# Optimization experiments

Measured on AMD Instinct MI355X. Metric: run time of the kernel, lower is better.

## Reference

```python
import jax, jax.numpy as jnp
import numpy as np
import math

B, S, D, H = 8, 1024, 512, 8  # batch, seqlen, d_model, heads
DK = D // H

def setup_inputs() -> dict:
    key = jax.random.key(0)
    ks = jax.random.split(key, 8)
    std = 1.0 / math.sqrt(D)
    return {
        "x": jax.random.normal(ks[0], (B, S, D), jnp.float32),
        "utT_similarities": jax.random.uniform(ks[1], (B, S, S), jnp.float32),
        "Wk": jax.random.normal(ks[2], (D, D), jnp.float32) * std,
        "bk": jnp.zeros((D,), jnp.float32),
        "Wv": jax.random.normal(ks[3], (D, D), jnp.float32) * std,
        "bv": jnp.zeros((D,), jnp.float32),
        "Wo": jax.random.normal(ks[4], (D, D), jnp.float32) * std,
        "bo": jnp.zeros((D,), jnp.float32),
        "gammas": jax.random.normal(ks[5], (H, 1, 1), jnp.float32) * 0.1,
    }

def reference(x, utT_similarities, Wk, bk, Wv, bv, Wo, bo, gammas):
    b, s, d = x.shape
    h = gammas.shape[0]
    dk = d // h
    NEG = -1e32

    def split_heads(t):  # [b,s,d] -> [b,h,s,dk]
        return t.reshape(b, s, h, dk).transpose(0, 2, 1, 3)

    # kq_same=True: q and k share k_linear
    q = split_heads(x @ Wk.T + bk)
    k = q
    v = split_heads(x @ Wv.T + bv)

    scores = jnp.einsum('bhid,bhjd->bhij', q, k) / jnp.sqrt(jnp.float32(dk))
    scores = scores * utT_similarities[:, None, :, :]

    mask = jnp.tril(jnp.ones((s, s), dtype=bool))  # causal, incl diagonal (mask=1)

    # distance-decay block (no_grad in torch -> stop_gradient)
    s_ = jax.nn.softmax(jnp.where(mask, scores, NEG), axis=-1) * mask
    distcum = jnp.cumsum(s_, axis=-1)
    disttotal = jnp.sum(s_, axis=-1, keepdims=True)
    idx = jnp.arange(s)
    position_effect = jnp.abs(idx[None, :] - idx[:, None]).astype(jnp.float32)  # [s,s]
    dist_scores = jnp.sqrt(jnp.clip((disttotal - distcum) * position_effect, 0.0, None))
    dist_scores = jax.lax.stop_gradient(dist_scores)

    gamma = -jax.nn.softplus(gammas)[None]  # [1,h,1,1]
    total_effect = jnp.clip(jnp.exp(dist_scores * gamma), 1e-5, 1e5)

    scores = jax.nn.softmax(jnp.where(mask, scores * total_effect, NEG), axis=-1)
    # zero_pad=False (mask=1 path), dropout is identity in eval
    out = jnp.einsum('bhij,bhjd->bhid', scores, v)
    out = out.transpose(0, 2, 1, 3).reshape(b, s, d)
    return out @ Wo.T + bo
```

## Files before the change

### kernel.cpp

```cpp
#include <hip/hip_runtime.h>
#include <math.h>

#define NB   8
#define SS   1024
#define DD   512
#define HH   8
#define DKK  64
#define NEGF (-3.0e38f)

#define QSTR 88
#define SSTR 257
#define PSTR 280

typedef _Float16 half8 __attribute__((ext_vector_type(8)));
typedef float    f32x4 __attribute__((ext_vector_type(4)));

#define GLDS16(g, l) __builtin_amdgcn_global_load_lds( \
    (const __attribute__((address_space(1))) void*)(g), \
    (__attribute__((address_space(3))) void*)(l), 16, 0, 0)

__global__ __launch_bounds__(256) void cvt_fp16(
    const float* __restrict__ x,  _Float16* __restrict__ xh,
    const float* __restrict__ wk, _Float16* __restrict__ wkh,
    const float* __restrict__ wv, _Float16* __restrict__ wvh,
    const float* __restrict__ wo, _Float16* __restrict__ woh)
{
    const size_t NX = (size_t)NB * SS * DD;
    const size_t NW = (size_t)DD * DD;
    size_t f = ((size_t)blockIdx.x * 256 + threadIdx.x) * 8;
    const float* src; _Float16* dst; size_t off;
    if (f < NX)               { src = x;  dst = xh;  off = f; }
    else if (f < NX + NW)     { src = wk; dst = wkh; off = f - NX; }
    else if (f < NX + 2*NW)   { src = wv; dst = wvh; off = f - NX - 2*NW + NW; }
    else                      { src = wo; dst = woh; off = f - NX - 2*NW; }
    float4 f0 = *(const float4*)&src[off];
    float4 f1 = *(const float4*)&src[off + 4];
    half8 hv = {(_Float16)f0.x,(_Float16)f0.y,(_Float16)f0.z,(_Float16)f0.w,
                (_Float16)f1.x,(_Float16)f1.y,(_Float16)f1.z,(_Float16)f1.w};
    *(half8*)&dst[off] = hv;
}

__global__ __launch_bounds__(256) void gemm_qv(
    const _Float16* __restrict__ xh,
    const _Float16* __restrict__ wkh, const float* __restrict__ bk,
    const _Float16* __restrict__ wvh, const float* __restrict__ bv,
    _Float16* __restrict__ q_ws, _Float16* __restrict__ vt_ws)
{
    __shared__ __align__(16) _Float16 Ah[128 * 32];
    __shared__ __align__(16) _Float16 Bh[128 * 32];

    const int m0  = blockIdx.x * 128;
    const int n0c = blockIdx.y * 128;
    const bool is_v = (n0c >= DD);
    const _Float16* __restrict__ Wp = is_v ? wvh : wkh;
    const float*    __restrict__ bp = is_v ? bv : bk;
    const int n0 = n0c & (DD - 1);

    const int tid  = threadIdx.x;
    const int w    = tid >> 6;
    const int lane = tid & 63;
    const int quad = lane >> 4;
    const int n    = lane & 15;
    const int wm   = w >> 1, wn = w & 1;

    const int ci0 = (w * 2 + 0) * 64 + lane;
    const int ci1 = (w * 2 + 1) * 64 + lane;
    const int r0c = ci0 >> 2, c0c = (ci0 & 3) * 8;
    const int r1c = ci1 >> 2, c1c = (ci1 & 3) * 8;
    _Float16* ldsA0 = &Ah[(w * 2 + 0) * 512];
    _Float16* ldsA1 = &Ah[(w * 2 + 1) * 512];
    _Float16* ldsB0 = &Bh[(w * 2 + 0) * 512];
    _Float16* ldsB1 = &Bh[(w * 2 + 1) * 512];

    f32x4 acc[4][4] = {};

    for (int k0 = 0; k0 < DD; k0 += 32) {
        __syncthreads();
        GLDS16(&xh[(size_t)(m0 + r0c) * DD + k0 + c0c], ldsA0);
        GLDS16(&xh[(size_t)(m0 + r1c) * DD + k0 + c1c], ldsA1);
        GLDS16(&Wp[(size_t)(n0 + r0c) * DD + k0 + c0c], ldsB0);
        GLDS16(&Wp[(size_t)(n0 + r1c) * DD + k0 + c1c], ldsB1);
        __syncthreads();
        half8 af[4], bf[4];
        #pragma unroll
        for (int mi = 0; mi < 4; ++mi)
            af[mi] = *(const half8*)&Ah[(wm*64 + mi*16 + n) * 32 + quad*8];
        #pragma unroll
        for (int ni = 0; ni < 4; ++ni)
            bf[ni] = *(const half8*)&Bh[(wn*64 + ni*16 + n) * 32 + quad*8];
        #pragma unroll
        for (int mi = 0; mi < 4; ++mi)
            #pragma unroll
            for (int ni = 0; ni < 4; ++ni)
                acc[mi][ni] = __builtin_amdgcn_mfma_f32_16x16x32_f16(
                    af[mi], bf[ni], acc[mi][ni], 0, 0, 0);
    }

    #pragma unroll
    for (int mi = 0; mi < 4; ++mi) {
        #pragma unroll
        for (int ni = 0; ni < 4; ++ni) {
            const int col = n0 + wn*64 + ni*16 + n;
            const int h   = col >> 6;
            const int dk  = col & 63;
            const float bias = bp[col];
            const int gbase = m0 + wm*64 + mi*16 + quad*4;
            const int bidx  = gbase >> 10;
            const int sr    = gbase & (SS - 1);
            if (!is_v) {
                #pragma unroll
                for (int reg = 0; reg < 4; ++reg)
                    q_ws[((size_t)(bidx * HH + h) * SS + sr + reg) * DKK + dk] =
                        (_Float16)(acc[mi][ni][reg] + bias);
            } else {
                _Float16 h4[4];
                #pragma unroll
                for (int reg = 0; reg < 4; ++reg)
                    h4[reg] = (_Float16)(acc[mi][ni][reg] + bias);
                *(uint2*)&vt_ws[((size_t)(bidx * HH + h) * DKK + dk) * SS + sr] =
                    *(uint2*)h4;
            }
        }
    }
}

__global__ __launch_bounds__(256) void gemm_out(
    const _Float16* __restrict__ A,
    const _Float16* __restrict__ woh, const float* __restrict__ bo,
    float* __restrict__ out)
{
    __shared__ __align__(16) _Float16 Ah[128 * 32];
    __shared__ __align__(16) _Float16 Bh[128 * 32];

    const int m0 = blockIdx.x * 128;
    const int n0 = blockIdx.y * 128;

    const int tid  = threadIdx.x;
    const int w    = tid >> 6;
    const int lane = tid & 63;
    const int quad = lane >> 4;
    const int n    = lane & 15;
    const int wm   = w >> 1, wn = w & 1;

    const int ci0 = (w * 2 + 0) * 64 + lane;
    const int ci1 = (w * 2 + 1) * 64 + lane;
    const int r0c = ci0 >> 2, c0c = (ci0 & 3) * 8;
    const int r1c = ci1 >> 2, c1c = (ci1 & 3) * 8;
    _Float16* ldsA0 = &Ah[(w * 2 + 0) * 512];
    _Float16* ldsA1 = &Ah[(w * 2 + 1) * 512];
    _Float16* ldsB0 = &Bh[(w * 2 + 0) * 512];
    _Float16* ldsB1 = &Bh[(w * 2 + 1) * 512];

    f32x4 acc[4][4] = {};

    for (int k0 = 0; k0 < DD; k0 += 32) {
        __syncthreads();
        GLDS16(&A[(size_t)(m0 + r0c) * DD + k0 + c0c], ldsA0);
        GLDS16(&A[(size_t)(m0 + r1c) * DD + k0 + c1c], ldsA1);
        GLDS16(&woh[(size_t)(n0 + r0c) * DD + k0 + c0c], ldsB0);
        GLDS16(&woh[(size_t)(n0 + r1c) * DD + k0 + c1c], ldsB1);
        __syncthreads();
        half8 af[4], bf[4];
        #pragma unroll
        for (int mi = 0; mi < 4; ++mi)
            af[mi] = *(const half8*)&Ah[(wm*64 + mi*16 + n) * 32 + quad*8];
        #pragma unroll
        for (int ni = 0; ni < 4; ++ni)
            bf[ni] = *(const half8*)&Bh[(wn*64 + ni*16 + n) * 32 + quad*8];
        #pragma unroll
        for (int mi = 0; mi < 4; ++mi)
            #pragma unroll
            for (int ni = 0; ni < 4; ++ni)
                acc[mi][ni] = __builtin_amdgcn_mfma_f32_16x16x32_f16(
                    af[mi], bf[ni], acc[mi][ni], 0, 0, 0);
    }

    #pragma unroll
    for (int mi = 0; mi < 4; ++mi) {
        #pragma unroll
        for (int ni = 0; ni < 4; ++ni) {
            const int col  = n0 + wn*64 + ni*16 + n;
            const float bias = bo[col];
            const int gbase = m0 + wm*64 + mi*16 + quad*4;
            #pragma unroll
            for (int reg = 0; reg < 4; ++reg)
                out[(size_t)(gbase + reg) * DD + col] = acc[mi][ni][reg] + bias;
        }
    }
}

__global__ __launch_bounds__(1024) void attn_mfma(
    const _Float16* __restrict__ q,
    const _Float16* __restrict__ vt,
    const float* __restrict__ utT,
    const float* __restrict__ gammas,
    _Float16* __restrict__ attn)
{
    __shared__ __align__(16) float    s_lds[2 * 16 * SSTR];
    __shared__ __align__(16) _Float16 q_lds[16 * QSTR];
    _Float16* p_lds = (_Float16*)s_lds;

    const int tid  = threadIdx.x;
    const int w    = tid >> 6;
    const int lane = tid & 63;
    const int quad = lane >> 4;
    const int n    = lane & 15;
    const int bh   = blockIdx.y;
    const int b    = bh >> 3;
    const int h    = bh & 7;
    const int r0   = blockIdx.x * 16;

    const _Float16* __restrict__ kq  = q  + (size_t)bh * SS * DKK;
    const _Float16* __restrict__ vtp = vt + (size_t)bh * DKK * SS;

    const int nchunk = (r0 + 16 + 255) >> 8;
    const int nt     = nchunk * 4;

    if (tid < 256) {
        const int row = tid >> 4;
        const int c   = tid & 15;
        *(uint2*)&q_lds[row * QSTR + c * 4] =
            *(const uint2*)&kq[(size_t)(r0 + row) * DKK + c * 4];
    }
    __syncthreads();

    float sreg[16];
    #pragma unroll
    for (int t2 = 0; t2 < 16; ++t2) sreg[t2] = NEGF;

    #pragma unroll
    for (int c0 = 0; c0 < 4; ++c0) {
        if (c0 < nchunk) {
            const int j0  = c0 * 256;
            const int buf = (c0 & 1) * 16 * SSTR;
            const int jbase = j0 + w * 16;
            if (jbase <= r0 + 15) {
                const _Float16* krow = &kq[(size_t)(jbase + n) * DKK];
                half8 b0 = *(const half8*)&krow[quad * 8];
                half8 b1 = *(const half8*)&krow[32 + quad * 8];
                half8 a0 = *(const half8*)&q_lds[n * QSTR + quad * 8];
                half8 a1 = *(const half8*)&q_lds[n * QSTR + 32 + quad * 8];
                f32x4 d = {0.f, 0.f, 0.f, 0.f};
                d = __builtin_amdgcn_mfma_f32_16x16x32_f16(a0, b0, d, 0, 0, 0);
                d = __builtin_amdgcn_mfma_f32_16x16x32_f16(a1, b1, d, 0, 0, 0);
                const int j = jbase + n;
                #pragma unroll
                for (int reg = 0; reg < 4; ++reg) {
                    const int i = r0 + quad * 4 + reg;
                    float val = NEGF;
                    if (j <= i)
                        val = d[reg] * 0.125f * utT[((size_t)b * SS + i) * SS + j];
                    s_lds[buf + (quad * 4 + reg) * SSTR + w * 16 + n] = val;
                }
            } else {
                #pragma unroll
                for (int reg = 0; reg < 4; ++reg)
                    s_lds[buf + (quad * 4 + reg) * SSTR + w * 16 + n] = NEGF;
            }
            __syncthreads();
            #pragma unroll
            for (int ttl = 0; ttl < 4; ++ttl)
                sreg[c0 * 4 + ttl] = s_lds[buf + w * SSTR + ttl * 64 + lane];
        }
    }

    const int i_row = r0 + w;

    float m1 = NEGF;
    #pragma unroll
    for (int t2 = 0; t2 < 16; ++t2) if (t2 < nt) m1 = fmaxf(m1, sreg[t2]);
    #pragma unroll
    for (int o = 32; o >= 1; o >>= 1) m1 = fmaxf(m1, __shfl_xor(m1, o));

    float ee[16];
    float z1 = 0.f;
    #pragma unroll
    for (int t2 = 0; t2 < 16; ++t2) {
        float e = 0.f;
        if (t2 < nt) {
            const int j = t2 * 64 + lane;
            if (j <= i_row) e = __expf(sreg[t2] - m1);
        }
        ee[t2] = e;
        z1 += e;
    }
    #pragma unroll
    for (int o = 32; o >= 1; o >>= 1) z1 += __shfl_xor(z1, o);
    const float inv_z1 = 1.0f / z1;

    const float g     = gammas[h];
    const float gamma = -log1pf(__expf(g));

    float carry = 0.f;
    float m2 = NEGF;
    #pragma unroll
    for (int t2 = 0; t2 < 16; ++t2) {
        if (t2 < nt) {
            float xv = ee[t2];
            #pragma unroll
            for (int o = 1; o < 64; o <<= 1) {
                float y = __shfl_up(xv, (unsigned)o);
                if (lane >= o) xv += y;
            }
            const float tile_tot = __shfl(xv, 63);
            const float csum = (carry + xv) * inv_z1;
            carry += tile_tot;

            const int j = t2 * 64 + lane;
            const float pe = (float)(i_row - j);
            const float dd = fmaxf((1.0f - csum) * pe, 0.0f);
            float te = __expf(sqrtf(dd) * gamma);
            te = fminf(fmaxf(te, 1e-5f), 1e5f);
            const float nsv = (j <= i_row) ? sreg[t2] * te : NEGF;
            ee[t2] = nsv;
            m2 = fmaxf(m2, nsv);
        }
    }
    #pragma unroll
    for (int o = 32; o >= 1; o >>= 1) m2 = fmaxf(m2, __shfl_xor(m2, o));

    float z2 = 0.f;
    #pragma unroll
    for (int t2 = 0; t2 < 16; ++t2) {
        if (t2 < nt) {
            ee[t2] = __expf(ee[t2] - m2);
            z2 += ee[t2];
        }
    }
    #pragma unroll
    for (int o = 32; o >= 1; o >>= 1) z2 += __shfl_xor(z2, o);
    const float inv_z2 = 1.0f / z2;
    #pragma unroll
    for (int t2 = 0; t2 < 16; ++t2) if (t2 < nt) ee[t2] *= inv_z2;

    __syncthreads();

    f32x4 oacc = {0.f, 0.f, 0.f, 0.f};
    #pragma unroll
    for (int c0 = 0; c0 < 4; ++c0) {
        if (c0 < nchunk) {
            const int j0 = c0 * 256;
            const int pb = (c0 & 1) * 16 * PSTR;
            #pragma unroll
            for (int ttl = 0; ttl < 4; ++ttl)
                p_lds[pb + w * PSTR + ttl * 64 + lane] = (_Float16)ee[c0 * 4 + ttl];
            __syncthreads();
            if (w < 4) {
                int nkt = (r0 + 16 - j0 + 31) >> 5;
                nkt = (nkt > 8) ? 8 : nkt;
                const _Float16* vrow = &vtp[(size_t)(w * 16 + n) * SS + j0];
                for (int kt = 0; kt < nkt; ++kt) {
                    half8 a  = *(const half8*)&p_lds[pb + n * PSTR + kt * 32 + quad * 8];
                    half8 bb = *(const half8*)&vrow[kt * 32 + quad * 8];
                    oacc = __builtin_amdgcn_mfma_f32_16x16x32_f16(a, bb, oacc, 0, 0, 0);
                }
            }
        }
    }

    if (w < 4) {
        #pragma unroll
        for (int reg = 0; reg < 4; ++reg) {
            const int i = r0 + quad * 4 + reg;
            attn[(((size_t)b * SS + i) * HH + h) * DKK + w * 16 + n] =
                (_Float16)oacc[reg];
        }
    }
}

extern "C" void kernel_launch(void* const* d_in, const int* in_sizes, int n_in,
                              void* d_out, int out_size, void* d_ws, size_t ws_size,
                              hipStream_t stream) {
    const float* x      = (const float*)d_in[0];
    const float* utT    = (const float*)d_in[1];
    const float* Wk     = (const float*)d_in[2];
    const float* bk     = (const float*)d_in[3];
    const float* Wv     = (const float*)d_in[4];
    const float* bv     = (const float*)d_in[5];
    const float* Wo     = (const float*)d_in[6];
    const float* bo     = (const float*)d_in[7];
    const float* gammas = (const float*)d_in[8];
    float* out = (float*)d_out;

    const size_t NX  = (size_t)NB * SS * DD;
    const size_t NW  = (size_t)DD * DD;
    const size_t per = NX;

    _Float16* p      = (_Float16*)d_ws;
    _Float16* xh     = p;  p += NX;
    _Float16* wkh    = p;  p += NW;
    _Float16* wvh    = p;  p += NW;
    _Float16* woh    = p;  p += NW;
    _Float16* q_ws   = p;  p += per;
    _Float16* vt_ws  = p;  p += per;
    _Float16* attn_h = p;  p += per;

    const int cvt_blocks = (int)((NX + 3 * NW) / 8 / 256);
    cvt_fp16<<<cvt_blocks, dim3(256), 0, stream>>>(
        x, xh, Wk, wkh, Wv, wvh, Wo, woh);

    dim3 g1(64, 8);
    gemm_qv<<<g1, dim3(256), 0, stream>>>(xh, wkh, bk, wvh, bv, q_ws, vt_ws);

    dim3 g2(SS / 16, NB * HH);
    attn_mfma<<<g2, dim3(1024), 0, stream>>>(q_ws, vt_ws, utT, gammas, attn_h);

    dim3 g3(64, 4);
    gemm_out<<<g3, dim3(256), 0, stream>>>(attn_h, woh, bo, out);
}
```

Baseline: 332.2 us.

## Use DPP wave scans and reductions, reverse row-block order, trim per-row tiles

The shuffle-based 64-lane prefix scan and the max/sum reductions become DPP row_shr, row_bcast, quad_perm and row_ror sequences plus readlane, which cuts LDS-backed shuffle traffic in the two-pass softmax. Row blocks are issued in reverse order, so the longest causal rows are scheduled first for better tail balance. Each wave now processes only the 64-column tiles up to its own diagonal and drops the per-element causal checks. The exp and sqrt use native exp2/sqrt builtins, and the redundant upper clamp is removed. These changes rely on masked scores being a huge negative value so they underflow to zero, and they slightly change rounding.

Result: faster. 292.5 us (-12.0%).

```diff
diff --git a/kernel.cpp b/kernel.cpp
--- a/kernel.cpp
+++ b/kernel.cpp
@@ -18,6 +18,48 @@
 #define GLDS16(g, l) __builtin_amdgcn_global_load_lds( \
     (const __attribute__((address_space(1))) void*)(g), \
     (__attribute__((address_space(3))) void*)(l), 16, 0, 0)
+
+template<int CTRL, int RM, int BM, bool BC>
+__device__ __forceinline__ float dpp_f(float x) {
+    return __builtin_bit_cast(float,
+        __builtin_amdgcn_update_dpp(0, __builtin_bit_cast(int, x),
+                                    CTRL, RM, BM, BC));
+}
+
+__device__ __forceinline__ float scan64(float x) {
+    x += dpp_f<0x111, 0xf, 0xf, true >(x);
+    x += dpp_f<0x112, 0xf, 0xf, true >(x);
+    x += dpp_f<0x114, 0xf, 0xf, true >(x);
+    x += dpp_f<0x118, 0xf, 0xf, true >(x);
+    x += dpp_f<0x142, 0xa, 0xf, false>(x);
+    x += dpp_f<0x143, 0xc, 0xf, false>(x);
+    return x;
+}
+
+__device__ __forceinline__ float redsum64(float x) {
+    x += dpp_f<0xB1,  0xf, 0xf, true>(x);
+    x += dpp_f<0x4E,  0xf, 0xf, true>(x);
+    x += dpp_f<0x141, 0xf, 0xf, true>(x);
+    x += dpp_f<0x140, 0xf, 0xf, true>(x);
+    x += __shfl_xor(x, 16);
+    x += __shfl_xor(x, 32);
+    return x;
+}
+
+__device__ __forceinline__ float redmax64(float x) {
+    x = fmaxf(x, dpp_f<0xB1,  0xf, 0xf, false>(x));
+    x = fmaxf(x, dpp_f<0x4E,  0xf, 0xf, false>(x));
+    x = fmaxf(x, dpp_f<0x141, 0xf, 0xf, false>(x));
+    x = fmaxf(x, dpp_f<0x140, 0xf, 0xf, false>(x));
+    x = fmaxf(x, __shfl_xor(x, 16));
+    x = fmaxf(x, __shfl_xor(x, 32));
+    return x;
+}
+
+__device__ __forceinline__ float bcast63(float x) {
+    return __builtin_bit_cast(float,
+        __builtin_amdgcn_readlane(__builtin_bit_cast(int, x), 63));
+}
 
 __global__ __launch_bounds__(256) void cvt_fp16(
     const float* __restrict__ x,  _Float16* __restrict__ xh,
@@ -208,7 +250,7 @@
     const int bh   = blockIdx.y;
     const int b    = bh >> 3;
     const int h    = bh & 7;
-    const int r0   = blockIdx.x * 16;
+    const int r0   = ((SS / 16 - 1) - blockIdx.x) * 16;
 
     const _Float16* __restrict__ kq  = q  + (size_t)bh * SS * DKK;
     const _Float16* __restrict__ vtp = vt + (size_t)bh * DKK * SS;
@@ -265,73 +307,63 @@
     }
 
     const int i_row = r0 + w;
+    const int ntw_u = (i_row >> 6) + 1;
+    const int ntw   = (nt < ntw_u) ? nt : ntw_u;
 
     float m1 = NEGF;
     #pragma unroll
-    for (int t2 = 0; t2 < 16; ++t2) if (t2 < nt) m1 = fmaxf(m1, sreg[t2]);
-    #pragma unroll
-    for (int o = 32; o >= 1; o >>= 1) m1 = fmaxf(m1, __shfl_xor(m1, o));
+    for (int t2 = 0; t2 < 16; ++t2) if (t2 < ntw) m1 = fmaxf(m1, sreg[t2]);
+    m1 = redmax64(m1);
 
     float ee[16];
     float z1 = 0.f;
     #pragma unroll
     for (int t2 = 0; t2 < 16; ++t2) {
         float e = 0.f;
-        if (t2 < nt) {
-            const int j = t2 * 64 + lane;
-            if (j <= i_row) e = __expf(sreg[t2] - m1);
-        }
+        if (t2 < ntw) e = __expf(sreg[t2] - m1);
         ee[t2] = e;
         z1 += e;
     }
-    #pragma unroll
-    for (int o = 32; o >= 1; o >>= 1) z1 += __shfl_xor(z1, o);
+    z1 = redsum64(z1);
     const float inv_z1 = 1.0f / z1;
 
-    const float g     = gammas[h];
-    const float gamma = -log1pf(__expf(g));
+    const float g   = gammas[h];
+    const float gl2 = -log1pf(__expf(g)) * 1.4426950408889634f;
 
     float carry = 0.f;
     float m2 = NEGF;
     #pragma unroll
     for (int t2 = 0; t2 < 16; ++t2) {
-        if (t2 < nt) {
-            float xv = ee[t2];
-            #pragma unroll
-            for (int o = 1; o < 64; o <<= 1) {
-                float y = __shfl_up(xv, (unsigned)o);
-                if (lane >= o) xv += y;
-            }
-            const float tile_tot = __shfl(xv, 63);
+        if (t2 < ntw) {
+            float xv = scan64(ee[t2]);
+            const float tile_tot = bcast63(xv);
             const float csum = (carry + xv) * inv_z1;
             carry += tile_tot;
 
             const int j = t2 * 64 + lane;
             const float pe = (float)(i_row - j);
             const float dd = fmaxf((1.0f - csum) * pe, 0.0f);
-            float te = __expf(sqrtf(dd) * gamma);
-            te = fminf(fmaxf(te, 1e-5f), 1e5f);
-            const float nsv = (j <= i_row) ? sreg[t2] * te : NEGF;
+            float te = __builtin_amdgcn_exp2f(__builtin_amdgcn_sqrtf(dd) * gl2);
+            te = fmaxf(te, 1e-5f);
+            const float nsv = sreg[t2] * te;
             ee[t2] = nsv;
             m2 = fmaxf(m2, nsv);
         }
     }
-    #pragma unroll
-    for (int o = 32; o >= 1; o >>= 1) m2 = fmaxf(m2, __shfl_xor(m2, o));
+    m2 = redmax64(m2);
 
     float z2 = 0.f;
     #pragma unroll
     for (int t2 = 0; t2 < 16; ++t2) {
-        if (t2 < nt) {
+        if (t2 < ntw) {
             ee[t2] = __expf(ee[t2] - m2);
             z2 += ee[t2];
         }
     }
-    #pragma unroll
-    for (int o = 32; o >= 1; o >>= 1) z2 += __shfl_xor(z2, o);
+    z2 = redsum64(z2);
     const float inv_z2 = 1.0f / z2;
     #pragma unroll
-    for (int t2 = 0; t2 < 16; ++t2) if (t2 < nt) ee[t2] *= inv_z2;
+    for (int t2 = 0; t2 < 16; ++t2) if (t2 < ntw) ee[t2] *= inv_z2;
 
     __syncthreads();
 
```
